# Performance work log

Hardware: AMD Instinct MI355X
Metric: run time of the kernel (lower is better)

Reference implementation:

```python
import jax, jax.numpy as jnp
import numpy as np

BATCH = 131072
N_ACTIONS = 512
EPSILON = 0.05


def setup_inputs() -> dict:
    key = jax.random.key(0)
    k1, k2, k3 = jax.random.split(key, 3)
    q_vals = jax.random.normal(k1, (BATCH, N_ACTIONS), dtype=jnp.float32)
    rand_u = jax.random.uniform(k2, (BATCH,), dtype=jnp.float32)
    rand_actions = jax.random.randint(k3, (BATCH,), 0, N_ACTIONS, dtype=jnp.int32)
    return {"q_vals": q_vals, "rand_u": rand_u, "rand_actions": rand_actions}


def reference(q_vals, rand_u, rand_actions):
    # Greedy actions: argmax over Q-values per sample.
    greedy = jnp.argmax(q_vals, axis=1).astype(jnp.int32)  # [B]
    # Epsilon-greedy override: where uniform < epsilon, use random action.
    explore = rand_u < EPSILON  # [B] bool
    return jnp.where(explore, rand_actions, greedy)
```

## Files before the change

kernel.cpp:

```cpp
#include <hip/hip_runtime.h>


#define N_ACTIONS 512
#define EPSILON 0.05f
#define ROWS_PER_BLOCK 4

__global__ __launch_bounds__(256) void
SelectAction_64862596104471_kernel(const float* __restrict__ q_vals,
                                   const float* __restrict__ rand_u,
                                   const int* __restrict__ rand_actions,
                                   int* __restrict__ out,
                                   int batch) {
    const int wave = threadIdx.x >> 6;
    const int lane = threadIdx.x & 63;
    const long long row = (long long)blockIdx.x * ROWS_PER_BLOCK + wave;
    if (row >= batch) return;

    const float4* qrow = (const float4*)(q_vals + row * (long long)N_ACTIONS);

    float4 a = qrow[lane];
    float4 b = qrow[lane + 64];

    float best = a.x;
    int bidx = 4 * lane;
    if (a.y > best) { best = a.y; bidx = 4 * lane + 1; }
    if (a.z > best) { best = a.z; bidx = 4 * lane + 2; }
    if (a.w > best) { best = a.w; bidx = 4 * lane + 3; }
    if (b.x > best) { best = b.x; bidx = 256 + 4 * lane; }
    if (b.y > best) { best = b.y; bidx = 256 + 4 * lane + 1; }
    if (b.z > best) { best = b.z; bidx = 256 + 4 * lane + 2; }
    if (b.w > best) { best = b.w; bidx = 256 + 4 * lane + 3; }

    #pragma unroll
    for (int off = 32; off > 0; off >>= 1) {
        float oval = __shfl_xor(best, off, 64);
        int oidx = __shfl_xor(bidx, off, 64);
        if (oval > best || (oval == best && oidx < bidx)) {
            best = oval;
            bidx = oidx;
        }
    }

    if (lane == 0) {
        const float u = rand_u[row];
        const int ra = rand_actions[row];
        out[row] = (u < EPSILON) ? ra : bidx;
    }
}

extern "C" void kernel_launch(void* const* d_in, const int* in_sizes, int n_in,
                              void* d_out, int out_size, void* d_ws, size_t ws_size,
                              hipStream_t stream) {
    const float* q_vals = (const float*)d_in[0];
    const float* rand_u = (const float*)d_in[1];
    const int* rand_actions = (const int*)d_in[2];
    int* out = (int*)d_out;

    const int batch = in_sizes[1];

    const int blocks = (batch + ROWS_PER_BLOCK - 1) / ROWS_PER_BLOCK;
    SelectAction_64862596104471_kernel<<<blocks, 256, 0, stream>>>(
        q_vals, rand_u, rand_actions, out, batch);
}
```

Baseline: 348.2 us.

## Process sixteen rows per wave with one-row-ahead prefetch

Each wave now loops over 16 consecutive rows, loading the next row's Q-values while reducing the current row. This shrinks the grid and aims to overlap global loads with the shuffle reduction while amortising block launch cost. The trade-off is fewer independent waves and a serial per-wave loop, which may reduce the number of memory requests in flight.

```diff
diff --git a/kernel.cpp b/kernel.cpp
--- a/kernel.cpp
+++ b/kernel.cpp
@@ -3,7 +3,9 @@
 
 #define N_ACTIONS 512
 #define EPSILON 0.05f
-#define ROWS_PER_BLOCK 4
+#define ROWS_PER_WAVE 16
+#define WAVES_PER_BLOCK 4
+#define ROWS_PER_BLOCK (ROWS_PER_WAVE * WAVES_PER_BLOCK)
 
 __global__ __launch_bounds__(256) void
 SelectAction_64862596104471_kernel(const float* __restrict__ q_vals,
@@ -11,40 +13,54 @@
                                    const int* __restrict__ rand_actions,
                                    int* __restrict__ out,
                                    int batch) {
-    const int wave = threadIdx.x >> 6;
     const int lane = threadIdx.x & 63;
-    const long long row = (long long)blockIdx.x * ROWS_PER_BLOCK + wave;
-    if (row >= batch) return;
+    const long long wave = (long long)blockIdx.x * WAVES_PER_BLOCK + (threadIdx.x >> 6);
+    const long long row0 = wave * ROWS_PER_WAVE;
+    if (row0 >= batch) return;
 
-    const float4* qrow = (const float4*)(q_vals + row * (long long)N_ACTIONS);
+    long long rem = (long long)batch - row0;
+    const int nrows = (rem < ROWS_PER_WAVE) ? (int)rem : ROWS_PER_WAVE;
 
-    float4 a = qrow[lane];
-    float4 b = qrow[lane + 64];
+    const float4* q = (const float4*)q_vals + row0 * (N_ACTIONS / 4);
 
-    float best = a.x;
-    int bidx = 4 * lane;
-    if (a.y > best) { best = a.y; bidx = 4 * lane + 1; }
-    if (a.z > best) { best = a.z; bidx = 4 * lane + 2; }
-    if (a.w > best) { best = a.w; bidx = 4 * lane + 3; }
-    if (b.x > best) { best = b.x; bidx = 256 + 4 * lane; }
-    if (b.y > best) { best = b.y; bidx = 256 + 4 * lane + 1; }
-    if (b.z > best) { best = b.z; bidx = 256 + 4 * lane + 2; }
-    if (b.w > best) { best = b.w; bidx = 256 + 4 * lane + 3; }
+    float4 a = q[lane];
+    float4 b = q[lane + 64];
 
-    #pragma unroll
-    for (int off = 32; off > 0; off >>= 1) {
-        float oval = __shfl_xor(best, off, 64);
-        int oidx = __shfl_xor(bidx, off, 64);
-        if (oval > best || (oval == best && oidx < bidx)) {
-            best = oval;
-            bidx = oidx;
+    for (int r = 0; r < nrows; ++r) {
+        float4 na = a, nb = b;
+        if (r + 1 < nrows) {
+            const float4* qn = q + (long long)(r + 1) * (N_ACTIONS / 4);
+            na = qn[lane];
+            nb = qn[lane + 64];
         }
-    }
 
-    if (lane == 0) {
-        const float u = rand_u[row];
-        const int ra = rand_actions[row];
-        out[row] = (u < EPSILON) ? ra : bidx;
+        float best = a.x;
+        int bidx = 4 * lane;
+        if (a.y > best) { best = a.y; bidx = 4 * lane + 1; }
+        if (a.z > best) { best = a.z; bidx = 4 * lane + 2; }
+        if (a.w > best) { best = a.w; bidx = 4 * lane + 3; }
+        if (b.x > best) { best = b.x; bidx = 256 + 4 * lane; }
+        if (b.y > best) { best = b.y; bidx = 256 + 4 * lane + 1; }
+        if (b.z > best) { best = b.z; bidx = 256 + 4 * lane + 2; }
+        if (b.w > best) { best = b.w; bidx = 256 + 4 * lane + 3; }
+
+        #pragma unroll
+        for (int off = 32; off > 0; off >>= 1) {
+            float ov = __shfl_xor(best, off, 64);
+            int oi = __shfl_xor(bidx, off, 64);
+            if (ov > best || (ov == best && oi < bidx)) {
+                best = ov;
+                bidx = oi;
+            }
+        }
+
+        if (lane == 0) {
+            const long long row = row0 + r;
+            out[row] = (rand_u[row] < EPSILON) ? rand_actions[row] : bidx;
+        }
+
+        a = na;
+        b = nb;
     }
 }
 
```

After: 354.9 us, median of 2. About the same (+1.9%).
